# Performance work log

Hardware: AMD Instinct MI355X
Metric: run time of the kernel (lower is better)

## Reference

```python
import jax, jax.numpy as jnp
import numpy as np

B, S, E, H, V, C = 64, 512, 256, 128, 50000, 2


def setup_inputs() -> dict:
    key = jax.random.key(0)
    ks = jax.random.split(key, 12)
    sentences = jax.random.randint(ks[0], (B, S), 0, V, dtype=jnp.int32)
    # sparse binary adjacency (dependency-tree-like), float for bmm
    adj = (jax.random.uniform(ks[1], (B, S, S)) < 0.05).astype(jnp.float32)
    emb_table = jax.random.normal(ks[2], (V, E), dtype=jnp.float32) * 0.02
    W1 = jax.random.normal(ks[3], (H, E), dtype=jnp.float32) * 0.05
    b1 = jnp.zeros((H,), jnp.float32)
    W2 = jax.random.normal(ks[4], (H, H), dtype=jnp.float32) * 0.05
    b2 = jnp.zeros((H,), jnp.float32)
    W3 = jax.random.normal(ks[5], (H, H), dtype=jnp.float32) * 0.05
    b3 = jnp.zeros((H,), jnp.float32)
    Wp = jax.random.normal(ks[6], (C, H), dtype=jnp.float32) * 0.05
    bp = jnp.zeros((C,), jnp.float32)
    return {"sentences": sentences, "adj": adj, "emb_table": emb_table,
            "W1": W1, "b1": b1, "W2": W2, "b2": b2, "W3": W3, "b3": b3,
            "Wp": Wp, "bp": bp}


def reference(sentences, adj, emb_table, W1, b1, W2, b2, W3, b3, Wp, bp):
    # embedding lookup (dropout is eval-mode identity)
    h = emb_table[sentences]  # [B, S, E]
    # degree normalization term (self-loop adds +1)
    deg = jnp.sum(adj, axis=-1, keepdims=True) + 1.0  # [B, S, 1]
    for W, b in ((W1, b1), (W2, b2), (W3, b3)):
        agg = jnp.einsum('bst,btd->bsd', adj, h)  # bmm(adj, h)
        # layer(agg) + layer(h) == (agg + h) @ W^T + 2b  (shared weights)
        h = ((agg + h) @ W.T + 2.0 * b) / deg
        h = jax.nn.relu(h)
    # AdaptiveMaxPool1d(1) over sequence dim
    pooled = jnp.max(h, axis=1)  # [B, H]
    logits = pooled @ Wp.T + bp  # [B, C]
    return logits
```

## Files before the change

### kernel.cpp

```cpp
#include <hip/hip_runtime.h>
#include <hip/hip_bf16.h>

typedef unsigned short ushort_t;

#define B_ 64
#define S_ 512
#define E_ 256
#define H_ 128
#define M_ (B_ * S_)
#define CAP_ 128

__global__ void k_adjidx(const float* __restrict__ adj,
                         ushort_t* __restrict__ idxl,
                         int* __restrict__ nnz,
                         float* __restrict__ invdeg) {
    int row  = blockIdx.x * 4 + (threadIdx.x >> 6);
    int lane = threadIdx.x & 63;
    const float4* arow = (const float4*)(adj + (size_t)row * S_);
    ushort_t* dst = idxl + (size_t)row * CAP_;
    int total = 0;
    #pragma unroll
    for (int c = 0; c < 2; ++c) {
        float4 v = arow[c * 64 + lane];
        float f[4] = {v.x, v.y, v.z, v.w};
        #pragma unroll
        for (int j = 0; j < 4; ++j) {
            unsigned long long m = __ballot(f[j] != 0.0f);
            if (f[j] != 0.0f) {
                int pos = total + __popcll(m & ((1ull << lane) - 1ull));
                if (pos < CAP_) dst[pos] = (ushort_t)(c * 256 + lane * 4 + j);
            }
            total += __popcll(m);
        }
    }
    if (lane == 0) {
        nnz[row] = total < CAP_ ? total : CAP_;
        invdeg[row] = 1.0f / (float)(total + 1);
    }
}

template <int WSTRIDE, int XSTRIDE, bool GATHER, bool ADD>
__global__ __launch_bounds__(256, 2) void k_gemm(const float* __restrict__ X,
                                                 const int* __restrict__ sent,
                                                 const float* __restrict__ emb,
                                                 const float* __restrict__ W,
                                                 int kBase,
                                                 float* __restrict__ out) {
    __shared__ float Ws[128][68];
    __shared__ float Xs[4][16][36];
    int tid  = threadIdx.x;
    int wave = tid >> 6, lane = tid & 63;
    int rb       = blockIdx.x >> 1;
    int colBase  = (blockIdx.x & 1) * 64;
    int rowBase  = rb * 128 + wave * 32;

    {
        int j  = tid & 63;
        int kq = tid >> 6;
        const float* wp = W + (size_t)(colBase + j) * WSTRIDE + kBase + kq * 32;
        #pragma unroll
        for (int i = 0; i < 8; ++i) {
            float4 v = *(const float4*)(wp + i * 4);
            int k = kq * 32 + i * 4;
            Ws[k + 0][j] = v.x; Ws[k + 1][j] = v.y;
            Ws[k + 2][j] = v.z; Ws[k + 3][j] = v.w;
        }
    }

    int cc = lane & 15, rr = lane >> 4;
    int kg = lane & 3,  rowi = lane >> 2;

    const float* xs0;
    const float* xs1;
    if (GATHER) {
        xs0 = emb + (size_t)sent[rowBase + rowi]      * XSTRIDE + kBase + kg * 4;
        xs1 = emb + (size_t)sent[rowBase + rowi + 16] * XSTRIDE + kBase + kg * 4;
    } else {
        xs0 = X + (size_t)(rowBase + rowi)      * XSTRIDE + kBase + kg * 4;
        xs1 = X + (size_t)(rowBase + rowi + 16) * XSTRIDE + kBase + kg * 4;
    }
    float4 f0 = *(const float4*)(xs0);
    float4 f1 = *(const float4*)(xs1);

    __syncthreads();

    float acc[8][4] = {};
    float (*xsw)[36] = Xs[wave];

    #pragma unroll 1
    for (int kk = 0; kk < 128; kk += 16) {
        xsw[kg * 4 + 0][rowi] = f0.x; xsw[kg * 4 + 1][rowi] = f0.y;
        xsw[kg * 4 + 2][rowi] = f0.z; xsw[kg * 4 + 3][rowi] = f0.w;
        xsw[kg * 4 + 0][rowi + 16] = f1.x; xsw[kg * 4 + 1][rowi + 16] = f1.y;
        xsw[kg * 4 + 2][rowi + 16] = f1.z; xsw[kg * 4 + 3][rowi + 16] = f1.w;
        if (kk + 16 < 128) {
            f0 = *(const float4*)(xs0 + kk + 16);
            f1 = *(const float4*)(xs1 + kk + 16);
        }
        #pragma unroll
        for (int k = 0; k < 16; ++k) {
            float4 x0 = *(const float4*)&xsw[k][rr * 8];
            float4 x1 = *(const float4*)&xsw[k][rr * 8 + 4];
            float4 wv = *(const float4*)&Ws[kk + k][cc * 4];
            float xv[8] = {x0.x, x0.y, x0.z, x0.w, x1.x, x1.y, x1.z, x1.w};
            #pragma unroll
            for (int i = 0; i < 8; ++i) {
                acc[i][0] += xv[i] * wv.x;
                acc[i][1] += xv[i] * wv.y;
                acc[i][2] += xv[i] * wv.z;
                acc[i][3] += xv[i] * wv.w;
            }
        }
    }

    #pragma unroll
    for (int i = 0; i < 8; ++i) {
        int row = rowBase + rr * 8 + i;
        float* op = out + (size_t)row * H_ + colBase + cc * 4;
        float4 o = {acc[i][0], acc[i][1], acc[i][2], acc[i][3]};
        if (ADD) {
            float4 p = *(const float4*)op;
            o.x += p.x; o.y += p.y; o.z += p.z; o.w += p.w;
        }
        *(float4*)op = o;
    }
}

template <bool POOL>
__global__ __launch_bounds__(256) void k_aggf(const float* __restrict__ Y,
                                              const ushort_t* __restrict__ idxl,
                                              const int* __restrict__ nnz,
                                              const float* __restrict__ invdeg,
                                              const float* __restrict__ bias,
                                              float* __restrict__ out) {
    int x    = blockIdx.x;
    int xcd  = x & 7;
    int slot = x >> 3;
    int b    = xcd + 8 * (slot >> 6);
    int g    = slot & 63;
    int r    = threadIdx.x >> 5;
    int row  = b * S_ + g * 8 + r;
    int c    = threadIdx.x & 31;

    const float4* Y4 = (const float4*)Y;
    int n = nnz[row];
    const ushort_t* il = idxl + (size_t)row * CAP_;
    float4 acc = Y4[(size_t)row * 32 + c];
    float4 acc2 = {0.f, 0.f, 0.f, 0.f};
    size_t base = (size_t)b * S_ * 32;

    int i = 0;
    for (; i + 4 <= n; i += 4) {
        int t0 = il[i], t1 = il[i + 1], t2 = il[i + 2], t3 = il[i + 3];
        float4 v0 = Y4[base + (size_t)t0 * 32 + c];
        float4 v1 = Y4[base + (size_t)t1 * 32 + c];
        float4 v2 = Y4[base + (size_t)t2 * 32 + c];
        float4 v3 = Y4[base + (size_t)t3 * 32 + c];
        acc.x += v0.x + v1.x; acc.y += v0.y + v1.y;
        acc.z += v0.z + v1.z; acc.w += v0.w + v1.w;
        acc2.x += v2.x + v3.x; acc2.y += v2.y + v3.y;
        acc2.z += v2.z + v3.z; acc2.w += v2.w + v3.w;
    }
    for (; i < n; ++i) {
        int t = il[i];
        float4 v = Y4[base + (size_t)t * 32 + c];
        acc.x += v.x; acc.y += v.y; acc.z += v.z; acc.w += v.w;
    }
    acc.x += acc2.x; acc.y += acc2.y; acc.z += acc2.z; acc.w += acc2.w;

    float inv = invdeg[row];
    float4 bv = ((const float4*)bias)[c];
    float4 o;
    o.x = fmaxf((acc.x + 2.0f * bv.x) * inv, 0.0f);
    o.y = fmaxf((acc.y + 2.0f * bv.y) * inv, 0.0f);
    o.z = fmaxf((acc.z + 2.0f * bv.z) * inv, 0.0f);
    o.w = fmaxf((acc.w + 2.0f * bv.w) * inv, 0.0f);

    if (!POOL) {
        ((float4*)out)[(size_t)row * 32 + c] = o;
    } else {
        __shared__ float4 sm[8][33];
        sm[r][c] = o;
        __syncthreads();
        if (r == 0) {
            float4 m = sm[0][c];
            #pragma unroll
            for (int q = 1; q < 8; ++q) {
                float4 v = sm[q][c];
                m.x = fmaxf(m.x, v.x); m.y = fmaxf(m.y, v.y);
                m.z = fmaxf(m.z, v.z); m.w = fmaxf(m.w, v.w);
            }
            ((float4*)out)[((size_t)b * 64 + g) * 32 + c] = m;
        }
    }
}

__global__ void k_final(const float* __restrict__ pp,
                        const float* __restrict__ Wp,
                        const float* __restrict__ bp,
                        float* __restrict__ out) {
    int b = blockIdx.x, j = threadIdx.x;
    const float* p = pp + (size_t)b * 64 * H_ + j;
    float m = -1e30f;
    #pragma unroll 8
    for (int i = 0; i < 64; ++i) m = fmaxf(m, p[(size_t)i * H_]);
    float t0 = m * Wp[j];
    float t1 = m * Wp[H_ + j];
    #pragma unroll
    for (int off = 32; off > 0; off >>= 1) {
        t0 += __shfl_down(t0, off);
        t1 += __shfl_down(t1, off);
    }
    __shared__ float red[2][2];
    int wave = j >> 6, lane = j & 63;
    if (lane == 0) { red[0][wave] = t0; red[1][wave] = t1; }
    __syncthreads();
    if (j == 0) out[b * 2 + 0] = red[0][0] + red[0][1] + bp[0];
    if (j == 1) out[b * 2 + 1] = red[1][0] + red[1][1] + bp[1];
}

extern "C" void kernel_launch(void* const* d_in, const int* in_sizes, int n_in,
                              void* d_out, int out_size, void* d_ws, size_t ws_size,
                              hipStream_t stream) {
    const int*   sent = (const int*)d_in[0];
    const float* adj  = (const float*)d_in[1];
    const float* emb  = (const float*)d_in[2];
    const float* W1   = (const float*)d_in[3];
    const float* b1   = (const float*)d_in[4];
    const float* W2   = (const float*)d_in[5];
    const float* b2   = (const float*)d_in[6];
    const float* W3   = (const float*)d_in[7];
    const float* b3   = (const float*)d_in[8];
    const float* Wp   = (const float*)d_in[9];
    const float* bp   = (const float*)d_in[10];
    float* out = (float*)d_out;

    char* ws = (char*)d_ws;
    float*    bufA   = (float*)ws;
    float*    bufB   = (float*)(ws + (size_t)M_ * 256 * 4);
    float*    invdeg = (float*)(ws + (size_t)M_ * 512 * 4);
    int*      nnz    = (int*)(ws + (size_t)M_ * 512 * 4 + M_ * 4);
    ushort_t* idxl   = (ushort_t*)(ws + (size_t)M_ * 512 * 4 + M_ * 8);
    float*    pp     = (float*)(ws + (size_t)M_ * 512 * 4 + M_ * 8 + (size_t)M_ * CAP_ * 2);

    k_adjidx<<<M_ / 4, 256, 0, stream>>>(adj, idxl, nnz, invdeg);

    k_gemm<E_, E_, true, false><<<512, 256, 0, stream>>>(nullptr, sent, emb, W1, 0,   bufA);
    k_gemm<E_, E_, true, true ><<<512, 256, 0, stream>>>(nullptr, sent, emb, W1, 128, bufA);
    k_aggf<false><<<M_ / 8, 256, 0, stream>>>(bufA, idxl, nnz, invdeg, b1, bufB);

    k_gemm<H_, H_, false, false><<<512, 256, 0, stream>>>(bufB, nullptr, nullptr, W2, 0, bufA);
    k_aggf<false><<<M_ / 8, 256, 0, stream>>>(bufA, idxl, nnz, invdeg, b2, bufB);

    k_gemm<H_, H_, false, false><<<512, 256, 0, stream>>>(bufB, nullptr, nullptr, W3, 0, bufA);
    k_aggf<true><<<M_ / 8, 256, 0, stream>>>(bufA, idxl, nnz, invdeg, b3, pp);

    k_final<<<B_, H_, 0, stream>>>(pp, Wp, bp, out);
}
```

Before: 303.0 us.

## Stage per-batch feature chunks in LDS for sparse aggregation with chunked GEMM output

The GEMM now writes its output in a [batch][chunk of 32 cols][row][32] layout. Each aggregation block then loads one batch's 512x32 slab (64KB) into shared memory and performs the neighbor gathers from LDS instead of global memory. The pooling max is folded into the aggregation block, so k_final only applies the projection. This trades many scattered global gathers for one contiguous slab load, at the cost of 64KB LDS per block, which limits occupancy, and only 256 blocks in the grid.

```diff
diff --git a/kernel.cpp b/kernel.cpp
--- a/kernel.cpp
+++ b/kernel.cpp
@@ -9,6 +9,7 @@
 #define H_ 128
 #define M_ (B_ * S_)
 #define CAP_ 128
+
 
 __global__ void k_adjidx(const float* __restrict__ adj,
                          ushort_t* __restrict__ idxl,
@@ -113,10 +114,13 @@
         }
     }
 
+    int col   = colBase + cc * 4;
+    int chunk = col >> 5, jc = col & 31;
     #pragma unroll
     for (int i = 0; i < 8; ++i) {
         int row = rowBase + rr * 8 + i;
-        float* op = out + (size_t)row * H_ + colBase + cc * 4;
+        int bb  = row >> 9, r = row & 511;
+        float* op = out + (((size_t)bb * 4 + chunk) * 512 + r) * 32 + jc;
         float4 o = {acc[i][0], acc[i][1], acc[i][2], acc[i][3]};
         if (ADD) {
             float4 p = *(const float4*)op;
@@ -127,83 +131,90 @@
 }
 
 template <bool POOL>
-__global__ __launch_bounds__(256) void k_aggf(const float* __restrict__ Y,
+__global__ __launch_bounds__(512) void k_aggf(const float* __restrict__ Y,
                                               const ushort_t* __restrict__ idxl,
                                               const int* __restrict__ nnz,
                                               const float* __restrict__ invdeg,
                                               const float* __restrict__ bias,
                                               float* __restrict__ out) {
-    int x    = blockIdx.x;
-    int xcd  = x & 7;
-    int slot = x >> 3;
-    int b    = xcd + 8 * (slot >> 6);
-    int g    = slot & 63;
-    int r    = threadIdx.x >> 5;
-    int row  = b * S_ + g * 8 + r;
-    int c    = threadIdx.x & 31;
-
-    const float4* Y4 = (const float4*)Y;
-    int n = nnz[row];
-    const ushort_t* il = idxl + (size_t)row * CAP_;
-    float4 acc = Y4[(size_t)row * 32 + c];
-    float4 acc2 = {0.f, 0.f, 0.f, 0.f};
-    size_t base = (size_t)b * S_ * 32;
-
-    int i = 0;
-    for (; i + 4 <= n; i += 4) {
-        int t0 = il[i], t1 = il[i + 1], t2 = il[i + 2], t3 = il[i + 3];
-        float4 v0 = Y4[base + (size_t)t0 * 32 + c];
-        float4 v1 = Y4[base + (size_t)t1 * 32 + c];
-        float4 v2 = Y4[base + (size_t)t2 * 32 + c];
-        float4 v3 = Y4[base + (size_t)t3 * 32 + c];
-        acc.x += v0.x + v1.x; acc.y += v0.y + v1.y;
-        acc.z += v0.z + v1.z; acc.w += v0.w + v1.w;
-        acc2.x += v2.x + v3.x; acc2.y += v2.y + v3.y;
-        acc2.z += v2.z + v3.z; acc2.w += v2.w + v3.w;
-    }
-    for (; i < n; ++i) {
-        int t = il[i];
-        float4 v = Y4[base + (size_t)t * 32 + c];
-        acc.x += v.x; acc.y += v.y; acc.z += v.z; acc.w += v.w;
-    }
-    acc.x += acc2.x; acc.y += acc2.y; acc.z += acc2.z; acc.w += acc2.w;
-
-    float inv = invdeg[row];
-    float4 bv = ((const float4*)bias)[c];
-    float4 o;
-    o.x = fmaxf((acc.x + 2.0f * bv.x) * inv, 0.0f);
-    o.y = fmaxf((acc.y + 2.0f * bv.y) * inv, 0.0f);
-    o.z = fmaxf((acc.z + 2.0f * bv.z) * inv, 0.0f);
-    o.w = fmaxf((acc.w + 2.0f * bv.w) * inv, 0.0f);
-
-    if (!POOL) {
-        ((float4*)out)[(size_t)row * 32 + c] = o;
-    } else {
-        __shared__ float4 sm[8][33];
-        sm[r][c] = o;
+    __shared__ float slab[512 * 32];
+    float4* s4 = (float4*)slab;
+    int b = blockIdx.x >> 2, chunk = blockIdx.x & 3;
+
+    const float4* g4 = (const float4*)(Y + (((size_t)b * 4 + chunk) * 512) * 32);
+    #pragma unroll
+    for (int i = 0; i < 8; ++i) s4[threadIdx.x + i * 512] = g4[threadIdx.x + i * 512];
+    __syncthreads();
+
+    int lane = threadIdx.x & 63, wave = threadIdx.x >> 6;
+    int grp  = wave * 8 + (lane >> 3);
+    int j    = lane & 7;
+    float4 bv = ((const float4*)bias)[chunk * 8 + j];
+    bv.x *= 2.0f; bv.y *= 2.0f; bv.z *= 2.0f; bv.w *= 2.0f;
+
+    float4 vmax = {-1e30f, -1e30f, -1e30f, -1e30f};
+
+    #pragma unroll 1
+    for (int i = 0; i < 8; ++i) {
+        int r   = grp * 8 + i;
+        int row = b * S_ + r;
+        int n = nnz[row];
+        const ushort_t* il = idxl + (size_t)row * CAP_;
+        float4 acc = s4[r * 8 + j];
+        float4 acc2 = {0.f, 0.f, 0.f, 0.f};
+        int q = 0;
+        for (; q + 4 <= n; q += 4) {
+            int t0 = il[q], t1 = il[q + 1], t2 = il[q + 2], t3 = il[q + 3];
+            float4 v0 = s4[t0 * 8 + j];
+            float4 v1 = s4[t1 * 8 + j];
+            float4 v2 = s4[t2 * 8 + j];
+            float4 v3 = s4[t3 * 8 + j];
+            acc.x += v0.x + v1.x; acc.y += v0.y + v1.y;
+            acc.z += v0.z + v1.z; acc.w += v0.w + v1.w;
+            acc2.x += v2.x + v3.x; acc2.y += v2.y + v3.y;
+            acc2.z += v2.z + v3.z; acc2.w += v2.w + v3.w;
+        }
+        for (; q < n; ++q) {
+            float4 v = s4[il[q] * 8 + j];
+            acc.x += v.x; acc.y += v.y; acc.z += v.z; acc.w += v.w;
+        }
+        acc.x += acc2.x; acc.y += acc2.y; acc.z += acc2.z; acc.w += acc2.w;
+
+        float inv = invdeg[row];
+        float4 o;
+        o.x = fmaxf((acc.x + bv.x) * inv, 0.0f);
+        o.y = fmaxf((acc.y + bv.y) * inv, 0.0f);
+        o.z = fmaxf((acc.z + bv.z) * inv, 0.0f);
+        o.w = fmaxf((acc.w + bv.w) * inv, 0.0f);
+
+        if (!POOL) {
+            *(float4*)(out + (size_t)row * H_ + chunk * 32 + j * 4) = o;
+        } else {
+            vmax.x = fmaxf(vmax.x, o.x); vmax.y = fmaxf(vmax.y, o.y);
+            vmax.z = fmaxf(vmax.z, o.z); vmax.w = fmaxf(vmax.w, o.w);
+        }
+    }
+
+    if (POOL) {
         __syncthreads();
-        if (r == 0) {
-            float4 m = sm[0][c];
-            #pragma unroll
-            for (int q = 1; q < 8; ++q) {
-                float4 v = sm[q][c];
-                m.x = fmaxf(m.x, v.x); m.y = fmaxf(m.y, v.y);
-                m.z = fmaxf(m.z, v.z); m.w = fmaxf(m.w, v.w);
-            }
-            ((float4*)out)[((size_t)b * 64 + g) * 32 + c] = m;
-        }
-    }
-}
-
-__global__ void k_final(const float* __restrict__ pp,
+        s4[grp * 8 + j] = vmax;
+        __syncthreads();
+        if (threadIdx.x < 32) {
+            int c = threadIdx.x;
+            float m = -1e30f;
+            #pragma unroll 8
+            for (int g = 0; g < 64; ++g) m = fmaxf(m, slab[g * 32 + c]);
+            out[(size_t)b * H_ + chunk * 32 + c] = m;
+        }
+    }
+}
+
+__global__ void k_final(const float* __restrict__ pooled,
                         const float* __restrict__ Wp,
                         const float* __restrict__ bp,
                         float* __restrict__ out) {
     int b = blockIdx.x, j = threadIdx.x;
-    const float* p = pp + (size_t)b * 64 * H_ + j;
-    float m = -1e30f;
-    #pragma unroll 8
-    for (int i = 0; i < 64; ++i) m = fmaxf(m, p[(size_t)i * H_]);
+    float m = pooled[(size_t)b * H_ + j];
     float t0 = m * Wp[j];
     float t1 = m * Wp[H_ + j];
     #pragma unroll
@@ -241,19 +252,19 @@
     float*    invdeg = (float*)(ws + (size_t)M_ * 512 * 4);
     int*      nnz    = (int*)(ws + (size_t)M_ * 512 * 4 + M_ * 4);
     ushort_t* idxl   = (ushort_t*)(ws + (size_t)M_ * 512 * 4 + M_ * 8);
-    float*    pp     = (float*)(ws + (size_t)M_ * 512 * 4 + M_ * 8 + (size_t)M_ * CAP_ * 2);
+    float*    pooled = (float*)(ws + (size_t)M_ * 512 * 4 + M_ * 8 + (size_t)M_ * CAP_ * 2);
 
     k_adjidx<<<M_ / 4, 256, 0, stream>>>(adj, idxl, nnz, invdeg);
 
     k_gemm<E_, E_, true, false><<<512, 256, 0, stream>>>(nullptr, sent, emb, W1, 0,   bufA);
     k_gemm<E_, E_, true, true ><<<512, 256, 0, stream>>>(nullptr, sent, emb, W1, 128, bufA);
-    k_aggf<false><<<M_ / 8, 256, 0, stream>>>(bufA, idxl, nnz, invdeg, b1, bufB);
+    k_aggf<false><<<B_ * 4, 512, 0, stream>>>(bufA, idxl, nnz, invdeg, b1, bufB);
 
     k_gemm<H_, H_, false, false><<<512, 256, 0, stream>>>(bufB, nullptr, nullptr, W2, 0, bufA);
-    k_aggf<false><<<M_ / 8, 256, 0, stream>>>(bufA, idxl, nnz, invdeg, b2, bufB);
+    k_aggf<false><<<B_ * 4, 512, 0, stream>>>(bufA, idxl, nnz, invdeg, b2, bufB);
 
     k_gemm<H_, H_, false, false><<<512, 256, 0, stream>>>(bufB, nullptr, nullptr, W3, 0, bufA);
-    k_aggf<true><<<M_ / 8, 256, 0, stream>>>(bufA, idxl, nnz, invdeg, b3, pp);
-
-    k_final<<<B_, H_, 0, stream>>>(pp, Wp, bp, out);
-}
+    k_aggf<true><<<B_ * 4, 512, 0, stream>>>(bufA, idxl, nnz, invdeg, b3, pooled);
+
+    k_final<<<B_, H_, 0, stream>>>(pooled, Wp, bp, out);
+}
```

Measured after the change: 306.5 us. Within noise of the previous version (+1.2%).

## Fuse per-layer GEMM and sparse aggregation into one kernel with per-batch spin barrier

Applied to the files above, without the earlier changes.

Each GCN layer now runs as one kernel. Four blocks per batch compute the GEMM into a chunked Y layout, sync through a per-batch atomic flag spin barrier, then stage 16-column chunks of the batch's Y into LDS and do the neighbor gather from shared memory instead of global memory. Pooling moves to a separate k_pool kernel, and the number of launches drops. The risk is that the spin barrier requires all 4 blocks of a batch to be co-resident. The GEMM tile is also smaller, with 16 rows per wave and weights reloaded per column chunk.

```diff
diff --git a/kernel.cpp b/kernel.cpp
--- a/kernel.cpp
+++ b/kernel.cpp
@@ -10,10 +10,13 @@
 #define M_ (B_ * S_)
 #define CAP_ 128
 
+
 __global__ void k_adjidx(const float* __restrict__ adj,
                          ushort_t* __restrict__ idxl,
                          int* __restrict__ nnz,
-                         float* __restrict__ invdeg) {
+                         float* __restrict__ invdeg,
+                         int* __restrict__ flags) {
+    if (blockIdx.x == 0 && threadIdx.x < 256) flags[threadIdx.x] = 0;
     int row  = blockIdx.x * 4 + (threadIdx.x >> 6);
     int lane = threadIdx.x & 63;
     const float4* arow = (const float4*)(adj + (size_t)row * S_);
@@ -39,160 +42,152 @@
     }
 }
 
-template <int WSTRIDE, int XSTRIDE, bool GATHER, bool ADD>
-__global__ __launch_bounds__(256, 2) void k_gemm(const float* __restrict__ X,
-                                                 const int* __restrict__ sent,
-                                                 const float* __restrict__ emb,
-                                                 const float* __restrict__ W,
-                                                 int kBase,
-                                                 float* __restrict__ out) {
-    __shared__ float Ws[128][68];
-    __shared__ float Xs[4][16][36];
+template <int K, bool GATHER>
+__global__ __launch_bounds__(512) void k_layer(const float* __restrict__ Xin,
+                                               const int* __restrict__ sent,
+                                               const float* __restrict__ emb,
+                                               const float* __restrict__ W,
+                                               const float* __restrict__ bias,
+                                               const ushort_t* __restrict__ idxl,
+                                               const int* __restrict__ nnz,
+                                               const float* __restrict__ invdeg,
+                                               float* __restrict__ Y,
+                                               int* __restrict__ flag,
+                                               float* __restrict__ hout) {
+    __shared__ __align__(16) float lds[11264];
     int tid  = threadIdx.x;
     int wave = tid >> 6, lane = tid & 63;
-    int rb       = blockIdx.x >> 1;
-    int colBase  = (blockIdx.x & 1) * 64;
-    int rowBase  = rb * 128 + wave * 32;
-
-    {
-        int j  = tid & 63;
-        int kq = tid >> 6;
-        const float* wp = W + (size_t)(colBase + j) * WSTRIDE + kBase + kq * 32;
+    int b = blockIdx.x >> 2, q = blockIdx.x & 3;
+    int rowBase = b * 512 + q * 128 + wave * 16;
+
+    float* Ws = lds;
+    float* Xs = lds + 8704 + wave * 320;
+
+    int rr = lane >> 4, cc = lane & 15;
+    int xrow = lane & 15, xkg = lane >> 4;
+
+    const float* xbase;
+    if (GATHER) xbase = emb + (size_t)sent[rowBase + xrow] * K + xkg * 4;
+    else        xbase = Xin + (size_t)(rowBase + xrow) * K + xkg * 4;
+
+    constexpr int NKH = K / 128;
+
+    for (int ch = 0; ch < 2; ++ch) {
+        float acc[4][4] = {};
+        for (int kh = 0; kh < NKH; ++kh) {
+            __syncthreads();
+            {
+                int j  = tid & 63;
+                int k0 = (tid >> 6) * 16;
+                const float* wp = W + (size_t)(ch * 64 + j) * K + kh * 128 + k0;
+                #pragma unroll
+                for (int i = 0; i < 4; ++i) {
+                    float4 v = *(const float4*)(wp + i * 4);
+                    int k = k0 + i * 4;
+                    Ws[(k + 0) * 68 + j] = v.x; Ws[(k + 1) * 68 + j] = v.y;
+                    Ws[(k + 2) * 68 + j] = v.z; Ws[(k + 3) * 68 + j] = v.w;
+                }
+            }
+            __syncthreads();
+            const float* xp = xbase + kh * 128;
+            float4 f = *(const float4*)xp;
+            #pragma unroll 1
+            for (int kk = 0; kk < 128; kk += 16) {
+                Xs[(xkg * 4 + 0) * 20 + xrow] = f.x;
+                Xs[(xkg * 4 + 1) * 20 + xrow] = f.y;
+                Xs[(xkg * 4 + 2) * 20 + xrow] = f.z;
+                Xs[(xkg * 4 + 3) * 20 + xrow] = f.w;
+                if (kk + 16 < 128) f = *(const float4*)(xp + kk + 16);
+                #pragma unroll
+                for (int k = 0; k < 16; ++k) {
+                    float4 x  = *(const float4*)&Xs[k * 20 + rr * 4];
+                    float4 wv = *(const float4*)&Ws[(kk + k) * 68 + cc * 4];
+                    acc[0][0] += x.x * wv.x; acc[0][1] += x.x * wv.y;
+                    acc[0][2] += x.x * wv.z; acc[0][3] += x.x * wv.w;
+                    acc[1][0] += x.y * wv.x; acc[1][1] += x.y * wv.y;
+                    acc[1][2] += x.y * wv.z; acc[1][3] += x.y * wv.w;
+                    acc[2][0] += x.z * wv.x; acc[2][1] += x.z * wv.y;
+                    acc[2][2] += x.z * wv.z; acc[2][3] += x.z * wv.w;
+                    acc[3][0] += x.w * wv.x; acc[3][1] += x.w * wv.y;
+                    acc[3][2] += x.w * wv.z; acc[3][3] += x.w * wv.w;
+                }
+            }
+        }
+        int col   = ch * 64 + cc * 4;
+        int chunk = col >> 4, jo = col & 15;
         #pragma unroll
-        for (int i = 0; i < 8; ++i) {
-            float4 v = *(const float4*)(wp + i * 4);
-            int k = kq * 32 + i * 4;
-            Ws[k + 0][j] = v.x; Ws[k + 1][j] = v.y;
-            Ws[k + 2][j] = v.z; Ws[k + 3][j] = v.w;
-        }
-    }
-
-    int cc = lane & 15, rr = lane >> 4;
-    int kg = lane & 3,  rowi = lane >> 2;
-
-    const float* xs0;
-    const float* xs1;
-    if (GATHER) {
-        xs0 = emb + (size_t)sent[rowBase + rowi]      * XSTRIDE + kBase + kg * 4;
-        xs1 = emb + (size_t)sent[rowBase + rowi + 16] * XSTRIDE + kBase + kg * 4;
-    } else {
-        xs0 = X + (size_t)(rowBase + rowi)      * XSTRIDE + kBase + kg * 4;
-        xs1 = X + (size_t)(rowBase + rowi + 16) * XSTRIDE + kBase + kg * 4;
-    }
-    float4 f0 = *(const float4*)(xs0);
-    float4 f1 = *(const float4*)(xs1);
-
+        for (int i = 0; i < 4; ++i) {
+            int rq = q * 128 + wave * 16 + rr * 4 + i;
+            float4 o = {acc[i][0], acc[i][1], acc[i][2], acc[i][3]};
+            *(float4*)(Y + (((size_t)b * 8 + chunk) * 512 + rq) * 16 + jo) = o;
+        }
+    }
+
+    __threadfence();
     __syncthreads();
-
-    float acc[8][4] = {};
-    float (*xsw)[36] = Xs[wave];
-
-    #pragma unroll 1
-    for (int kk = 0; kk < 128; kk += 16) {
-        xsw[kg * 4 + 0][rowi] = f0.x; xsw[kg * 4 + 1][rowi] = f0.y;
-        xsw[kg * 4 + 2][rowi] = f0.z; xsw[kg * 4 + 3][rowi] = f0.w;
-        xsw[kg * 4 + 0][rowi + 16] = f1.x; xsw[kg * 4 + 1][rowi + 16] = f1.y;
-        xsw[kg * 4 + 2][rowi + 16] = f1.z; xsw[kg * 4 + 3][rowi + 16] = f1.w;
-        if (kk + 16 < 128) {
-            f0 = *(const float4*)(xs0 + kk + 16);
-            f1 = *(const float4*)(xs1 + kk + 16);
-        }
-        #pragma unroll
-        for (int k = 0; k < 16; ++k) {
-            float4 x0 = *(const float4*)&xsw[k][rr * 8];
-            float4 x1 = *(const float4*)&xsw[k][rr * 8 + 4];
-            float4 wv = *(const float4*)&Ws[kk + k][cc * 4];
-            float xv[8] = {x0.x, x0.y, x0.z, x0.w, x1.x, x1.y, x1.z, x1.w};
-            #pragma unroll
-            for (int i = 0; i < 8; ++i) {
-                acc[i][0] += xv[i] * wv.x;
-                acc[i][1] += xv[i] * wv.y;
-                acc[i][2] += xv[i] * wv.z;
-                acc[i][3] += xv[i] * wv.w;
-            }
-        }
-    }
-
-    #pragma unroll
-    for (int i = 0; i < 8; ++i) {
-        int row = rowBase + rr * 8 + i;
-        float* op = out + (size_t)row * H_ + colBase + cc * 4;
-        float4 o = {acc[i][0], acc[i][1], acc[i][2], acc[i][3]};
-        if (ADD) {
-            float4 p = *(const float4*)op;
-            o.x += p.x; o.y += p.y; o.z += p.z; o.w += p.w;
-        }
-        *(float4*)op = o;
-    }
-}
-
-template <bool POOL>
-__global__ __launch_bounds__(256) void k_aggf(const float* __restrict__ Y,
-                                              const ushort_t* __restrict__ idxl,
-                                              const int* __restrict__ nnz,
-                                              const float* __restrict__ invdeg,
-                                              const float* __restrict__ bias,
-                                              float* __restrict__ out) {
-    int x    = blockIdx.x;
-    int xcd  = x & 7;
-    int slot = x >> 3;
-    int b    = xcd + 8 * (slot >> 6);
-    int g    = slot & 63;
-    int r    = threadIdx.x >> 5;
-    int row  = b * S_ + g * 8 + r;
-    int c    = threadIdx.x & 31;
-
-    const float4* Y4 = (const float4*)Y;
+    if (tid == 0) {
+        atomicAdd(flag + b, 1);
+        while (__hip_atomic_load(flag + b, __ATOMIC_RELAXED,
+                                 __HIP_MEMORY_SCOPE_AGENT) < 4)
+            __builtin_amdgcn_s_sleep(2);
+    }
+    __syncthreads();
+    __threadfence();
+
+    float4* s4 = (float4*)lds;
+    int r   = tid >> 2;
+    int j   = tid & 3;
+    int row = b * 512 + q * 128 + r;
+    int rq  = q * 128 + r;
     int n = nnz[row];
     const ushort_t* il = idxl + (size_t)row * CAP_;
-    float4 acc = Y4[(size_t)row * 32 + c];
-    float4 acc2 = {0.f, 0.f, 0.f, 0.f};
-    size_t base = (size_t)b * S_ * 32;
-
-    int i = 0;
-    for (; i + 4 <= n; i += 4) {
-        int t0 = il[i], t1 = il[i + 1], t2 = il[i + 2], t3 = il[i + 3];
-        float4 v0 = Y4[base + (size_t)t0 * 32 + c];
-        float4 v1 = Y4[base + (size_t)t1 * 32 + c];
-        float4 v2 = Y4[base + (size_t)t2 * 32 + c];
-        float4 v3 = Y4[base + (size_t)t3 * 32 + c];
-        acc.x += v0.x + v1.x; acc.y += v0.y + v1.y;
-        acc.z += v0.z + v1.z; acc.w += v0.w + v1.w;
-        acc2.x += v2.x + v3.x; acc2.y += v2.y + v3.y;
-        acc2.z += v2.z + v3.z; acc2.w += v2.w + v3.w;
-    }
-    for (; i < n; ++i) {
-        int t = il[i];
-        float4 v = Y4[base + (size_t)t * 32 + c];
-        acc.x += v.x; acc.y += v.y; acc.z += v.z; acc.w += v.w;
-    }
-    acc.x += acc2.x; acc.y += acc2.y; acc.z += acc2.z; acc.w += acc2.w;
-
     float inv = invdeg[row];
-    float4 bv = ((const float4*)bias)[c];
-    float4 o;
-    o.x = fmaxf((acc.x + 2.0f * bv.x) * inv, 0.0f);
-    o.y = fmaxf((acc.y + 2.0f * bv.y) * inv, 0.0f);
-    o.z = fmaxf((acc.z + 2.0f * bv.z) * inv, 0.0f);
-    o.w = fmaxf((acc.w + 2.0f * bv.w) * inv, 0.0f);
-
-    if (!POOL) {
-        ((float4*)out)[(size_t)row * 32 + c] = o;
-    } else {
-        __shared__ float4 sm[8][33];
-        sm[r][c] = o;
+
+    #pragma unroll 1
+    for (int ch2 = 0; ch2 < 8; ++ch2) {
         __syncthreads();
-        if (r == 0) {
-            float4 m = sm[0][c];
-            #pragma unroll
-            for (int q = 1; q < 8; ++q) {
-                float4 v = sm[q][c];
-                m.x = fmaxf(m.x, v.x); m.y = fmaxf(m.y, v.y);
-                m.z = fmaxf(m.z, v.z); m.w = fmaxf(m.w, v.w);
-            }
-            ((float4*)out)[((size_t)b * 64 + g) * 32 + c] = m;
-        }
-    }
+        const float4* g4 = (const float4*)(Y + ((size_t)b * 8 + ch2) * 512 * 16);
+        #pragma unroll
+        for (int i = 0; i < 4; ++i) s4[tid + i * 512] = g4[tid + i * 512];
+        __syncthreads();
+
+        float4 acc = s4[rq * 4 + j];
+        float4 acc2 = {0.f, 0.f, 0.f, 0.f};
+        int t = 0;
+        for (; t + 4 <= n; t += 4) {
+            int t0 = il[t], t1 = il[t + 1], t2 = il[t + 2], t3 = il[t + 3];
+            float4 v0 = s4[t0 * 4 + j];
+            float4 v1 = s4[t1 * 4 + j];
+            float4 v2 = s4[t2 * 4 + j];
+            float4 v3 = s4[t3 * 4 + j];
+            acc.x += v0.x + v1.x; acc.y += v0.y + v1.y;
+            acc.z += v0.z + v1.z; acc.w += v0.w + v1.w;
+            acc2.x += v2.x + v3.x; acc2.y += v2.y + v3.y;
+            acc2.z += v2.z + v3.z; acc2.w += v2.w + v3.w;
+        }
+        for (; t < n; ++t) {
+            float4 v = s4[il[t] * 4 + j];
+            acc.x += v.x; acc.y += v.y; acc.z += v.z; acc.w += v.w;
+        }
+        acc.x += acc2.x; acc.y += acc2.y; acc.z += acc2.z; acc.w += acc2.w;
+
+        float4 bv = *(const float4*)(bias + ch2 * 16 + j * 4);
+        float4 o;
+        o.x = fmaxf((acc.x + 2.0f * bv.x) * inv, 0.0f);
+        o.y = fmaxf((acc.y + 2.0f * bv.y) * inv, 0.0f);
+        o.z = fmaxf((acc.z + 2.0f * bv.z) * inv, 0.0f);
+        o.w = fmaxf((acc.w + 2.0f * bv.w) * inv, 0.0f);
+        *(float4*)(hout + (size_t)row * H_ + ch2 * 16 + j * 4) = o;
+    }
+}
+
+__global__ void k_pool(const float* __restrict__ h, float* __restrict__ pp) {
+    int b = blockIdx.x >> 2, qq = blockIdx.x & 3, j = threadIdx.x;
+    const float* p = h + ((size_t)b * 512 + qq * 128) * H_ + j;
+    float m = -1e30f;
+    #pragma unroll 8
+    for (int s = 0; s < 128; ++s) m = fmaxf(m, p[(size_t)s * H_]);
+    pp[(size_t)blockIdx.x * H_ + j] = m;
 }
 
 __global__ void k_final(const float* __restrict__ pp,
@@ -200,10 +195,10 @@
                         const float* __restrict__ bp,
                         float* __restrict__ out) {
     int b = blockIdx.x, j = threadIdx.x;
-    const float* p = pp + (size_t)b * 64 * H_ + j;
-    float m = -1e30f;
-    #pragma unroll 8
-    for (int i = 0; i < 64; ++i) m = fmaxf(m, p[(size_t)i * H_]);
+    float m = pp[(size_t)(b * 4 + 0) * H_ + j];
+    m = fmaxf(m, pp[(size_t)(b * 4 + 1) * H_ + j]);
+    m = fmaxf(m, pp[(size_t)(b * 4 + 2) * H_ + j]);
+    m = fmaxf(m, pp[(size_t)(b * 4 + 3) * H_ + j]);
     float t0 = m * Wp[j];
     float t1 = m * Wp[H_ + j];
     #pragma unroll
@@ -236,24 +231,25 @@
     float* out = (float*)d_out;
 
     char* ws = (char*)d_ws;
-    float*    bufA   = (float*)ws;
-    float*    bufB   = (float*)(ws + (size_t)M_ * 256 * 4);
-    float*    invdeg = (float*)(ws + (size_t)M_ * 512 * 4);
-    int*      nnz    = (int*)(ws + (size_t)M_ * 512 * 4 + M_ * 4);
-    ushort_t* idxl   = (ushort_t*)(ws + (size_t)M_ * 512 * 4 + M_ * 8);
-    float*    pp     = (float*)(ws + (size_t)M_ * 512 * 4 + M_ * 8 + (size_t)M_ * CAP_ * 2);
-
-    k_adjidx<<<M_ / 4, 256, 0, stream>>>(adj, idxl, nnz, invdeg);
-
-    k_gemm<E_, E_, true, false><<<512, 256, 0, stream>>>(nullptr, sent, emb, W1, 0,   bufA);
-    k_gemm<E_, E_, true, true ><<<512, 256, 0, stream>>>(nullptr, sent, emb, W1, 128, bufA);
-    k_aggf<false><<<M_ / 8, 256, 0, stream>>>(bufA, idxl, nnz, invdeg, b1, bufB);
-
-    k_gemm<H_, H_, false, false><<<512, 256, 0, stream>>>(bufB, nullptr, nullptr, W2, 0, bufA);
-    k_aggf<false><<<M_ / 8, 256, 0, stream>>>(bufA, idxl, nnz, invdeg, b2, bufB);
-
-    k_gemm<H_, H_, false, false><<<512, 256, 0, stream>>>(bufB, nullptr, nullptr, W3, 0, bufA);
-    k_aggf<true><<<M_ / 8, 256, 0, stream>>>(bufA, idxl, nnz, invdeg, b3, pp);
-
-    k_final<<<B_, H_, 0, stream>>>(pp, Wp, bp, out);
-}
+    float* Ybuf = (float*)ws;
+    float* h2   = (float*)(ws + ((size_t)16 << 20));
+    float* h1   = (float*)(ws + ((size_t)32 << 20));
+    char*  base = ws + ((size_t)48 << 20);
+    float*    invdeg = (float*)base;
+    int*      nnz    = (int*)(base + (size_t)M_ * 4);
+    ushort_t* idxl   = (ushort_t*)(base + (size_t)M_ * 8);
+    float*    pp     = (float*)(base + (size_t)M_ * 8 + (size_t)M_ * CAP_ * 2);
+    int*      flags  = (int*)(base + (size_t)M_ * 8 + (size_t)M_ * CAP_ * 2 + 256 * H_ * 4);
+
+    k_adjidx<<<M_ / 4, 256, 0, stream>>>(adj, idxl, nnz, invdeg, flags);
+
+    k_layer<E_, true ><<<256, 512, 0, stream>>>(nullptr, sent, emb, W1, b1,
+                                                idxl, nnz, invdeg, Ybuf, flags + 0,   h1);
+    k_layer<H_, false><<<256, 512, 0, stream>>>(h1, nullptr, nullptr, W2, b2,
+                                                idxl, nnz, invdeg, Ybuf, flags + 64,  h2);
+    k_layer<H_, false><<<256, 512, 0, stream>>>(h2, nullptr, nullptr, W3, b3,
+                                                idxl, nnz, invdeg, Ybuf, flags + 128, h1);
+
+    k_pool <<<256, H_, 0, stream>>>(h1, pp);
+    k_final<<<B_,  H_, 0, stream>>>(pp, Wp, bp, out);
+}
```

Result: slower. 634.6 us (+109.4%).
